# Kernel tuning notes

Hardware: AMD Instinct MI355X
Metric: run time of the kernel (lower is better)

## Reference

```python
import jax, jax.numpy as jnp
import numpy as np

C = 256      # channels
G = 8        # groups
K = 9        # 3x3 sampling points (DCNv4 default kernel_size=3)
DWK = 3      # dw_kernel_size (wrapper passes kernel_size=3)
OFFSET_SCALE = 1.0
N, H, W = 8, 64, 64


def setup_inputs() -> dict:
    key = jax.random.key(0)
    ks = jax.random.split(key, 6)
    def init(k, shape, fan):
        return jax.random.normal(k, shape, jnp.float32) * (fan ** -0.5)
    return {
        "x": jax.random.normal(ks[0], (N, C, H, W), jnp.float32),
        "dw_w": init(ks[1], (C, 1, DWK, DWK), DWK * DWK),   # depthwise conv (OIHW, groups=C)
        "dw_b": jnp.zeros((C,), jnp.float32),
        "om_w": init(ks[2], (G * K * 3, C), C) * 0.01,       # offset/mask linear (small offsets)
        "om_b": jnp.zeros((G * K * 3,), jnp.float32),
        "vp_w": init(ks[3], (C, C), C),                      # value_proj
        "vp_b": jnp.zeros((C,), jnp.float32),
        "op_w": init(ks[4], (C, C), C),                      # output_proj (output_bias=False)
    }


def reference(x, dw_w, dw_b, om_w, om_b, vp_w, vp_b, op_w):
    n, c, h, w = x.shape
    cg = c // G
    L = h * w
    # b c h w -> b (h w) c
    xf = x.transpose(0, 2, 3, 1).reshape(n, L, c)
    value = (xf @ vp_w.T + vp_b).reshape(n, L, G, cg)
    # offset/mask branch: depthwise conv on raw input, then linear
    om_in = jax.lax.conv_general_dilated(
        x, dw_w, (1, 1), "SAME", feature_group_count=c,
        dimension_numbers=("NCHW", "OIHW", "NCHW")) + dw_b[None, :, None, None]
    om = om_in.transpose(0, 2, 3, 1).reshape(n, L, c) @ om_w.T + om_b  # (n, L, G*K*3)
    om = om.reshape(n, h, w, G, K * 3)
    off = om[..., : 2 * K].reshape(n, h, w, G, K, 2) * OFFSET_SCALE     # (dy, dx) per point
    mask = om[..., 2 * K:]                                              # (n,h,w,G,K) raw (DCNv4: no softmax)
    # base 3x3 dilation-1 grid centered at each pixel
    d = jnp.arange(-1, 2, dtype=jnp.float32)
    dy, dx = jnp.meshgrid(d, d, indexing="ij")
    base = jnp.stack([dy.ravel(), dx.ravel()], -1)  # (K, 2)
    py = (jnp.arange(h, dtype=jnp.float32).reshape(1, h, 1, 1, 1)
          + base[:, 0].reshape(1, 1, 1, 1, K) + off[..., 0])  # (n,h,w,G,K)
    px = (jnp.arange(w, dtype=jnp.float32).reshape(1, 1, w, 1, 1)
          + base[:, 1].reshape(1, 1, 1, 1, K) + off[..., 1])
    y0 = jnp.floor(py); x0 = jnp.floor(px)
    ty = py - y0; tx = px - x0
    y0i = y0.astype(jnp.int32); x0i = x0.astype(jnp.int32)

    def gather(yi, xi, wgt):
        valid = (yi >= 0) & (yi < h) & (xi >= 0) & (xi < w)
        idx = jnp.clip(yi, 0, h - 1) * w + jnp.clip(xi, 0, w - 1)       # (n,h,w,G,K)
        idx = idx.transpose(0, 1, 2, 4, 3).reshape(n, L * K, G)[..., None]
        g = jnp.take_along_axis(value, idx, axis=1)                     # (n, L*K, G, cg)
        g = g.reshape(n, h, w, K, G, cg).transpose(0, 1, 2, 4, 3, 5)    # (n,h,w,G,K,cg)
        return g * (wgt * valid)[..., None]

    sampled = (gather(y0i,     x0i,     (1 - ty) * (1 - tx))
             + gather(y0i,     x0i + 1, (1 - ty) * tx)
             + gather(y0i + 1, x0i,     ty * (1 - tx))
             + gather(y0i + 1, x0i + 1, ty * tx))
    out = jnp.einsum("nhwgk,nhwgkc->nhwgc", mask, sampled)  # mask-weighted aggregation
    out = out.reshape(n, L, c) @ op_w.T                      # output_proj (no bias)
    # b (h w) c -> b c h w
    return out.reshape(n, h, w, c).transpose(0, 3, 1, 2)
```

## Files before the change

kernel.cpp:

```cpp
#include <hip/hip_runtime.h>
#include <math.h>

#define N_  8
#define C_  256
#define G_  8
#define CG_ 32
#define K_  9
#define H_  64
#define W_  64
#define L_  (H_*W_)
#define OM_ 216
#define OMP_ 256

using frag_ab = __attribute__((ext_vector_type(8))) short;
using frag_cd = __attribute__((ext_vector_type(4))) float;

__device__ __forceinline__ unsigned short f2bf(float f) {
    unsigned int u = __float_as_uint(f);
    u += 0x7FFFu + ((u >> 16) & 1u);
    return (unsigned short)(u >> 16);
}
__device__ __forceinline__ float bflo(unsigned int u) { return __uint_as_float(u << 16); }
__device__ __forceinline__ float bfhi(unsigned int u) { return __uint_as_float(u & 0xFFFF0000u); }

__device__ __forceinline__ void gld16(const void* g, void* l) {
    __builtin_amdgcn_global_load_lds((const __attribute__((address_space(1))) void*)g,
                                     (__attribute__((address_space(3))) void*)l, 16, 0, 0);
}

__global__ __launch_bounds__(256) void cvt_weights(const float* __restrict__ vp_w,
                                                   const float* __restrict__ om_w,
                                                   const float* __restrict__ om_b,
                                                   const float* __restrict__ op_w,
                                                   unsigned short* __restrict__ vp_wb,
                                                   unsigned short* __restrict__ om_wb,
                                                   float* __restrict__ om_bp,
                                                   unsigned short* __restrict__ op_wb) {
    int idx = blockIdx.x * 256 + threadIdx.x;
    if (idx < C_ * C_) {
        vp_wb[idx] = f2bf(vp_w[idx]);
        op_wb[idx] = f2bf(op_w[idx]);
        om_wb[idx] = (idx < OM_ * C_) ? f2bf(om_w[idx]) : (unsigned short)0;
    }
    if (idx < OMP_) om_bp[idx] = (idx < OM_) ? om_b[idx] : 0.f;
}

__global__ __launch_bounds__(256) void dwt_kernel(const float* __restrict__ x,
                                                  const float* __restrict__ w,
                                                  const float* __restrict__ b,
                                                  unsigned short* __restrict__ omb) {
    const int n = blockIdx.z, y = blockIdx.y, c0 = blockIdx.x * 32;
    const int tid = threadIdx.x;
    __shared__ float xs[3][32][66];
    if (tid < 192) {
        int r = tid / 64, c = (tid / 2) % 32, e = tid & 1;
        xs[r][c][e * 65] = 0.f;
    }
    const float* xb = x + ((size_t)n * C_ + c0) * L_;
    for (int i = tid; i < 3 * 32 * 16; i += 256) {
        int r = i >> 9;
        int rem = i & 511;
        int c = rem >> 4;
        int x4 = (rem & 15) * 4;
        int yy = y + r - 1;
        float4 v = make_float4(0.f, 0.f, 0.f, 0.f);
        if ((unsigned)yy < (unsigned)H_) v = *(const float4*)(xb + (size_t)c * L_ + yy * W_ + x4);
        xs[r][c][1 + x4] = v.x; xs[r][c][2 + x4] = v.y;
        xs[r][c][3 + x4] = v.z; xs[r][c][4 + x4] = v.w;
    }
    __syncthreads();

    const int c = tid & 31, x0 = (tid >> 5) * 8;
    float wv[9];
#pragma unroll
    for (int i = 0; i < 9; i++) wv[i] = w[(c0 + c) * 9 + i];
    const float bias = b[c0 + c];
    float o[8];
#pragma unroll
    for (int j = 0; j < 8; j++) o[j] = bias;
#pragma unroll
    for (int r = 0; r < 3; r++) {
        float v[10];
#pragma unroll
        for (int d = 0; d < 10; d++) v[d] = xs[r][c][x0 + d];
#pragma unroll
        for (int j = 0; j < 8; j++)
            o[j] += wv[r * 3] * v[j] + wv[r * 3 + 1] * v[j + 1] + wv[r * 3 + 2] * v[j + 2];
    }
#pragma unroll
    for (int j = 0; j < 8; j++)
        omb[((size_t)n * L_ + y * W_ + x0 + j) * C_ + c0 + c] = f2bf(o[j]);
}

__global__ __launch_bounds__(256) void xcvt_kernel(const float* __restrict__ x,
                                                   unsigned short* __restrict__ xb) {
    const int n = blockIdx.z, c0 = blockIdx.y * 32, l0 = blockIdx.x * 64;
    const int tid = threadIdx.x;
    __shared__ float t[32][65];
    {
        int c = tid >> 3, l8 = (tid & 7) * 8;
        const float* src = x + ((size_t)n * C_ + c0 + c) * L_ + l0 + l8;
        float4 a = *(const float4*)src;
        float4 d = *(const float4*)(src + 4);
        t[c][l8 + 0] = a.x; t[c][l8 + 1] = a.y; t[c][l8 + 2] = a.z; t[c][l8 + 3] = a.w;
        t[c][l8 + 4] = d.x; t[c][l8 + 5] = d.y; t[c][l8 + 6] = d.z; t[c][l8 + 7] = d.w;
    }
    __syncthreads();
    {
        int l = tid >> 2, cq = (tid & 3) * 8;
        uint4 pk;
        unsigned short* pp = (unsigned short*)&pk;
#pragma unroll
        for (int i = 0; i < 8; i++) pp[i] = f2bf(t[cq + i][l]);
        *(uint4*)(xb + ((size_t)n * L_ + l0 + l) * C_ + c0 + cq) = pk;
    }
}

template <bool BF16_OUT, bool BIAS>
__global__ __launch_bounds__(256) void gemm_bf16(const unsigned short* __restrict__ A,
                                                 const unsigned short* __restrict__ B,
                                                 const float* __restrict__ bias,
                                                 void* __restrict__ Dv,
                                                 int drow, long bbatch, long dbatch) {
    __shared__ unsigned short As[128 * 32];
    __shared__ unsigned short Bs[128 * 32];
    const int tid = threadIdx.x;
    const long i0 = (long)blockIdx.x * 128;
    const long j0 = (long)blockIdx.y * 128;
    const unsigned short* Ab = A + i0 * C_;
    const unsigned short* Bb = B + bbatch * blockIdx.z + j0 * C_;
    const int wave = tid >> 6, lane = tid & 63;
    const int iw = (wave & 1) * 64, jw = (wave >> 1) * 64;
    const int lm = lane & 15, kq = lane >> 4;
    const int srow = tid >> 2, scol = (tid & 3) * 8;

    frag_cd acc[4][4];
#pragma unroll
    for (int a = 0; a < 4; a++)
#pragma unroll
        for (int c = 0; c < 4; c++) acc[a][c] = (frag_cd){0.f, 0.f, 0.f, 0.f};

    for (int k0 = 0; k0 < C_; k0 += 32) {
        const unsigned short* ga0 = Ab + (long)srow * C_ + k0 + scol;
        const unsigned short* gb0 = Bb + (long)srow * C_ + k0 + scol;
        gld16(ga0,            As + tid * 8);
        gld16(ga0 + 64 * C_,  As + 2048 + tid * 8);
        gld16(gb0,            Bs + tid * 8);
        gld16(gb0 + 64 * C_,  Bs + 2048 + tid * 8);
        __syncthreads();
        frag_ab af[4], bfr[4];
#pragma unroll
        for (int mi = 0; mi < 4; mi++)
            af[mi] = *(const frag_ab*)&As[(iw + mi * 16 + lm) * 32 + kq * 8];
#pragma unroll
        for (int ni = 0; ni < 4; ni++)
            bfr[ni] = *(const frag_ab*)&Bs[(jw + ni * 16 + lm) * 32 + kq * 8];
#pragma unroll
        for (int mi = 0; mi < 4; mi++)
#pragma unroll
            for (int ni = 0; ni < 4; ni++)
                acc[mi][ni] = __builtin_amdgcn_mfma_f32_16x16x32_bf16(af[mi], bfr[ni], acc[mi][ni], 0, 0, 0);
        __syncthreads();
    }

    float bv[4];
#pragma unroll
    for (int ni = 0; ni < 4; ni++)
        bv[ni] = BIAS ? bias[(int)(j0 + jw + ni * 16 + lm)] : 0.f;

    const long ibase = i0 + iw + kq * 4;
    const long jbase = j0 + jw + lm;
    const long dz = dbatch * blockIdx.z;
#pragma unroll
    for (int mi = 0; mi < 4; mi++) {
#pragma unroll
        for (int ni = 0; ni < 4; ni++) {
            long j = jbase + ni * 16;
#pragma unroll
            for (int r = 0; r < 4; r++) {
                long i = ibase + mi * 16 + r;
                float v = acc[mi][ni][r] + bv[ni];
                if (BF16_OUT)
                    ((unsigned short*)Dv)[dz + i * drow + j] = f2bf(v);
                else
                    ((float*)Dv)[dz + i * drow + j] = v;
            }
        }
    }
}

__global__ __launch_bounds__(256) void sample_kernel(const unsigned short* __restrict__ value,
                                                     const float* __restrict__ om,
                                                     unsigned short* __restrict__ interm) {
    const int n = blockIdx.y;
    const int l0 = blockIdx.x * 8;
    const int tid = threadIdx.x;
    const int p = tid >> 5;
    const int l = l0 + p;
    const int y = l >> 6, xp = l & 63;
    const int g = (tid >> 2) & 7;
    const int c8 = (tid & 3) * 8;

    __shared__ float sOm[8 * OM_];
    const float* omsrc = om + ((size_t)n * L_ + l0) * OMP_;
    for (int i = tid; i < 8 * OM_; i += 256) {
        int pp = i / OM_;
        int j = i - pp * OM_;
        sOm[i] = omsrc[pp * OMP_ + j];
    }
    __syncthreads();

    const unsigned short* vb = value + (size_t)n * L_ * C_ + g * CG_ + c8;
    const float* so = &sOm[p * OM_ + g * 27];
    float acc[8] = {0.f, 0.f, 0.f, 0.f, 0.f, 0.f, 0.f, 0.f};
#pragma unroll
    for (int k = 0; k < K_; k++) {
        float offy = so[2 * k], offx = so[2 * k + 1], mk = so[18 + k];
        float py = (float)(y + k / 3 - 1) + offy;
        float px = (float)(xp + k % 3 - 1) + offx;
        float fy = floorf(py), fx = floorf(px);
        float ty = py - fy, tx = px - fx;
        int y0 = (int)fy, x0 = (int)fx;
        int y1 = y0 + 1, x1 = x0 + 1;
        float vy0 = ((unsigned)y0 < (unsigned)H_) ? 1.f : 0.f;
        float vy1 = ((unsigned)y1 < (unsigned)H_) ? 1.f : 0.f;
        float vx0 = ((unsigned)x0 < (unsigned)W_) ? 1.f : 0.f;
        float vx1 = ((unsigned)x1 < (unsigned)W_) ? 1.f : 0.f;
        int cy0 = min(max(y0, 0), H_ - 1), cy1 = min(max(y1, 0), H_ - 1);
        int cx0 = min(max(x0, 0), W_ - 1), cx1 = min(max(x1, 0), W_ - 1);
        float w00 = mk * (1.f - ty) * (1.f - tx) * vy0 * vx0;
        float w01 = mk * (1.f - ty) * tx * vy0 * vx1;
        float w10 = mk * ty * (1.f - tx) * vy1 * vx0;
        float w11 = mk * ty * tx * vy1 * vx1;
        const uint4 v00 = *(const uint4*)(vb + (size_t)(cy0 * W_ + cx0) * C_);
        const uint4 v01 = *(const uint4*)(vb + (size_t)(cy0 * W_ + cx1) * C_);
        const uint4 v10 = *(const uint4*)(vb + (size_t)(cy1 * W_ + cx0) * C_);
        const uint4 v11 = *(const uint4*)(vb + (size_t)(cy1 * W_ + cx1) * C_);
#define ACC8(V, WW) { \
        acc[0] += WW * bflo(V.x); acc[1] += WW * bfhi(V.x); \
        acc[2] += WW * bflo(V.y); acc[3] += WW * bfhi(V.y); \
        acc[4] += WW * bflo(V.z); acc[5] += WW * bfhi(V.z); \
        acc[6] += WW * bflo(V.w); acc[7] += WW * bfhi(V.w); }
        ACC8(v00, w00) ACC8(v01, w01) ACC8(v10, w10) ACC8(v11, w11)
#undef ACC8
    }
    uint4 pk;
    unsigned short* pp2 = (unsigned short*)&pk;
#pragma unroll
    for (int i = 0; i < 8; i++) pp2[i] = f2bf(acc[i]);
    *(uint4*)(interm + ((size_t)n * L_ + l) * C_ + g * CG_ + c8) = pk;
}

extern "C" void kernel_launch(void* const* d_in, const int* in_sizes, int n_in,
                              void* d_out, int out_size, void* d_ws, size_t ws_size,
                              hipStream_t stream) {
    const float* x    = (const float*)d_in[0];
    const float* dw_w = (const float*)d_in[1];
    const float* dw_b = (const float*)d_in[2];
    const float* om_w = (const float*)d_in[3];
    const float* om_b = (const float*)d_in[4];
    const float* vp_w = (const float*)d_in[5];
    const float* vp_b = (const float*)d_in[6];
    const float* op_w = (const float*)d_in[7];
    float* out = (float*)d_out;

    char* ws = (char*)d_ws;
    unsigned short* xb      = (unsigned short*)(ws);
    unsigned short* omb     = (unsigned short*)(ws + 16777216);
    unsigned short* valueb  = (unsigned short*)(ws + 33554432);
    float*          omf     = (float*)(ws + 50331648);
    unsigned short* vp_wb   = (unsigned short*)(ws + 83886080);
    unsigned short* om_wb   = (unsigned short*)(ws + 84017152);
    unsigned short* op_wb   = (unsigned short*)(ws + 84148224);
    float*          om_bp   = (float*)(ws + 84279296);
    unsigned short* intermb = xb;

    cvt_weights<<<dim3(256), 256, 0, stream>>>(vp_w, om_w, om_b, op_w,
                                               vp_wb, om_wb, om_bp, op_wb);
    dwt_kernel<<<dim3(C_ / 32, H_, N_), 256, 0, stream>>>(x, dw_w, dw_b, omb);
    xcvt_kernel<<<dim3(L_ / 64, C_ / 32, N_), 256, 0, stream>>>(x, xb);
    gemm_bf16<true, true><<<dim3(256, 2, 1), 256, 0, stream>>>(
        xb, vp_wb, vp_b, valueb, C_, 0, 0);
    gemm_bf16<false, true><<<dim3(256, 2, 1), 256, 0, stream>>>(
        omb, om_wb, om_bp, omf, OMP_, 0, 0);
    sample_kernel<<<dim3(L_ / 8, N_), 256, 0, stream>>>(valueb, omf, intermb);
    gemm_bf16<false, false><<<dim3(2, 32, N_), 256, 0, stream>>>(
        op_wb, intermb, nullptr, out, L_, (long)L_ * C_, (long)C_ * L_);
}
```

Before: 185.1 us.

## Fuse x bf16 transpose into depthwise conv kernel and precompute sampling weights

Merges the x-to-bf16 NHWC conversion into the depthwise conv kernel, reusing the center row already staged in shared memory, and stages both outputs through LDS so they can be written as 16-byte stores. This removes one kernel launch and a second full read of x. The sampling kernel now computes bilinear weights and byte offsets once per (pixel, group, point) into shared memory instead of redundantly in each of the 4 channel lanes, then gathers using those precomputed offsets. The cost is extra shared memory and an additional barrier in both kernels.

```diff
diff --git a/kernel.cpp b/kernel.cpp
--- a/kernel.cpp
+++ b/kernel.cpp
@@ -45,26 +45,25 @@
     if (idx < OMP_) om_bp[idx] = (idx < OM_) ? om_b[idx] : 0.f;
 }
 
-__global__ __launch_bounds__(256) void dwt_kernel(const float* __restrict__ x,
-                                                  const float* __restrict__ w,
-                                                  const float* __restrict__ b,
-                                                  unsigned short* __restrict__ omb) {
+__global__ __launch_bounds__(256) void prep_kernel(const float* __restrict__ x,
+                                                   const float* __restrict__ w,
+                                                   const float* __restrict__ b,
+                                                   unsigned short* __restrict__ xb,
+                                                   unsigned short* __restrict__ omb) {
     const int n = blockIdx.z, y = blockIdx.y, c0 = blockIdx.x * 32;
     const int tid = threadIdx.x;
     __shared__ float xs[3][32][66];
+    __shared__ __align__(16) unsigned short os[2][64][40];
     if (tid < 192) {
         int r = tid / 64, c = (tid / 2) % 32, e = tid & 1;
         xs[r][c][e * 65] = 0.f;
     }
-    const float* xb = x + ((size_t)n * C_ + c0) * L_;
+    const float* xbase = x + ((size_t)n * C_ + c0) * L_;
     for (int i = tid; i < 3 * 32 * 16; i += 256) {
-        int r = i >> 9;
-        int rem = i & 511;
-        int c = rem >> 4;
-        int x4 = (rem & 15) * 4;
+        int r = i >> 9, rem = i & 511, c = rem >> 4, x4 = (rem & 15) * 4;
         int yy = y + r - 1;
         float4 v = make_float4(0.f, 0.f, 0.f, 0.f);
-        if ((unsigned)yy < (unsigned)H_) v = *(const float4*)(xb + (size_t)c * L_ + yy * W_ + x4);
+        if ((unsigned)yy < (unsigned)H_) v = *(const float4*)(xbase + (size_t)c * L_ + yy * W_ + x4);
         xs[r][c][1 + x4] = v.x; xs[r][c][2 + x4] = v.y;
         xs[r][c][3 + x4] = v.z; xs[r][c][4 + x4] = v.w;
     }
@@ -88,32 +87,18 @@
             o[j] += wv[r * 3] * v[j] + wv[r * 3 + 1] * v[j + 1] + wv[r * 3 + 2] * v[j + 2];
     }
 #pragma unroll
-    for (int j = 0; j < 8; j++)
-        omb[((size_t)n * L_ + y * W_ + x0 + j) * C_ + c0 + c] = f2bf(o[j]);
-}
-
-__global__ __launch_bounds__(256) void xcvt_kernel(const float* __restrict__ x,
-                                                   unsigned short* __restrict__ xb) {
-    const int n = blockIdx.z, c0 = blockIdx.y * 32, l0 = blockIdx.x * 64;
-    const int tid = threadIdx.x;
-    __shared__ float t[32][65];
-    {
-        int c = tid >> 3, l8 = (tid & 7) * 8;
-        const float* src = x + ((size_t)n * C_ + c0 + c) * L_ + l0 + l8;
-        float4 a = *(const float4*)src;
-        float4 d = *(const float4*)(src + 4);
-        t[c][l8 + 0] = a.x; t[c][l8 + 1] = a.y; t[c][l8 + 2] = a.z; t[c][l8 + 3] = a.w;
-        t[c][l8 + 4] = d.x; t[c][l8 + 5] = d.y; t[c][l8 + 6] = d.z; t[c][l8 + 7] = d.w;
-    }
-    __syncthreads();
-    {
-        int l = tid >> 2, cq = (tid & 3) * 8;
-        uint4 pk;
-        unsigned short* pp = (unsigned short*)&pk;
-#pragma unroll
-        for (int i = 0; i < 8; i++) pp[i] = f2bf(t[cq + i][l]);
-        *(uint4*)(xb + ((size_t)n * L_ + l0 + l) * C_ + c0 + cq) = pk;
-    }
+    for (int j = 0; j < 8; j++) {
+        os[0][x0 + j][c] = f2bf(xs[1][c][1 + x0 + j]);
+        os[1][x0 + j][c] = f2bf(o[j]);
+    }
+    __syncthreads();
+
+    const int l = tid >> 2, c8 = (tid & 3) * 8;
+    uint4 va = *(const uint4*)&os[0][l][c8];
+    uint4 vc = *(const uint4*)&os[1][l][c8];
+    size_t dst = ((size_t)n * L_ + y * W_ + l) * C_ + c0 + c8;
+    *(uint4*)(xb + dst) = va;
+    *(uint4*)(omb + dst) = vc;
 }
 
 template <bool BF16_OUT, bool BIAS>
@@ -195,60 +180,71 @@
     const int n = blockIdx.y;
     const int l0 = blockIdx.x * 8;
     const int tid = threadIdx.x;
-    const int p = tid >> 5;
-    const int l = l0 + p;
-    const int y = l >> 6, xp = l & 63;
-    const int g = (tid >> 2) & 7;
-    const int c8 = (tid & 3) * 8;
 
     __shared__ float sOm[8 * OM_];
+    __shared__ float4 wgt[64][9];
+    __shared__ uint4  soff[64][9];
+
     const float* omsrc = om + ((size_t)n * L_ + l0) * OMP_;
     for (int i = tid; i < 8 * OM_; i += 256) {
         int pp = i / OM_;
-        int j = i - pp * OM_;
-        sOm[i] = omsrc[pp * OMP_ + j];
-    }
-    __syncthreads();
-
-    const unsigned short* vb = value + (size_t)n * L_ * C_ + g * CG_ + c8;
-    const float* so = &sOm[p * OM_ + g * 27];
-    float acc[8] = {0.f, 0.f, 0.f, 0.f, 0.f, 0.f, 0.f, 0.f};
-#pragma unroll
-    for (int k = 0; k < K_; k++) {
+        sOm[i] = omsrc[pp * OMP_ + (i - pp * OM_)];
+    }
+    __syncthreads();
+
+    for (int it = tid; it < 576; it += 256) {
+        int pair = it / 9, k = it - pair * 9;
+        int p = pair >> 3, g = pair & 7;
+        int l = l0 + p, y = l >> 6, xp2 = l & 63;
+        const float* so = &sOm[p * OM_ + g * 27];
         float offy = so[2 * k], offx = so[2 * k + 1], mk = so[18 + k];
         float py = (float)(y + k / 3 - 1) + offy;
-        float px = (float)(xp + k % 3 - 1) + offx;
+        float px = (float)(xp2 + k % 3 - 1) + offx;
         float fy = floorf(py), fx = floorf(px);
         float ty = py - fy, tx = px - fx;
-        int y0 = (int)fy, x0 = (int)fx;
-        int y1 = y0 + 1, x1 = x0 + 1;
+        int y0 = (int)fy, x0i = (int)fx;
+        int y1 = y0 + 1, x1 = x0i + 1;
         float vy0 = ((unsigned)y0 < (unsigned)H_) ? 1.f : 0.f;
         float vy1 = ((unsigned)y1 < (unsigned)H_) ? 1.f : 0.f;
-        float vx0 = ((unsigned)x0 < (unsigned)W_) ? 1.f : 0.f;
+        float vx0 = ((unsigned)x0i < (unsigned)W_) ? 1.f : 0.f;
         float vx1 = ((unsigned)x1 < (unsigned)W_) ? 1.f : 0.f;
         int cy0 = min(max(y0, 0), H_ - 1), cy1 = min(max(y1, 0), H_ - 1);
-        int cx0 = min(max(x0, 0), W_ - 1), cx1 = min(max(x1, 0), W_ - 1);
-        float w00 = mk * (1.f - ty) * (1.f - tx) * vy0 * vx0;
-        float w01 = mk * (1.f - ty) * tx * vy0 * vx1;
-        float w10 = mk * ty * (1.f - tx) * vy1 * vx0;
-        float w11 = mk * ty * tx * vy1 * vx1;
-        const uint4 v00 = *(const uint4*)(vb + (size_t)(cy0 * W_ + cx0) * C_);
-        const uint4 v01 = *(const uint4*)(vb + (size_t)(cy0 * W_ + cx1) * C_);
-        const uint4 v10 = *(const uint4*)(vb + (size_t)(cy1 * W_ + cx0) * C_);
-        const uint4 v11 = *(const uint4*)(vb + (size_t)(cy1 * W_ + cx1) * C_);
+        int cx0 = min(max(x0i, 0), W_ - 1), cx1 = min(max(x1, 0), W_ - 1);
+        wgt[pair][k] = make_float4(mk * (1.f - ty) * (1.f - tx) * vy0 * vx0,
+                                   mk * (1.f - ty) * tx         * vy0 * vx1,
+                                   mk * ty         * (1.f - tx) * vy1 * vx0,
+                                   mk * ty         * tx         * vy1 * vx1);
+        soff[pair][k] = make_uint4((unsigned)((cy0 * W_ + cx0) << 9),
+                                   (unsigned)((cy0 * W_ + cx1) << 9),
+                                   (unsigned)((cy1 * W_ + cx0) << 9),
+                                   (unsigned)((cy1 * W_ + cx1) << 9));
+    }
+    __syncthreads();
+
+    const int pair = tid >> 2, p = pair >> 3, g = pair & 7, c8 = (tid & 3) * 8;
+    const char* vb = (const char*)(value + (size_t)n * L_ * C_ + g * CG_ + c8);
+    float acc[8] = {0.f, 0.f, 0.f, 0.f, 0.f, 0.f, 0.f, 0.f};
+#pragma unroll
+    for (int k = 0; k < K_; k++) {
+        float4 wk = wgt[pair][k];
+        uint4  ok = soff[pair][k];
+        const uint4 v00 = *(const uint4*)(vb + ok.x);
+        const uint4 v01 = *(const uint4*)(vb + ok.y);
+        const uint4 v10 = *(const uint4*)(vb + ok.z);
+        const uint4 v11 = *(const uint4*)(vb + ok.w);
 #define ACC8(V, WW) { \
         acc[0] += WW * bflo(V.x); acc[1] += WW * bfhi(V.x); \
         acc[2] += WW * bflo(V.y); acc[3] += WW * bfhi(V.y); \
         acc[4] += WW * bflo(V.z); acc[5] += WW * bfhi(V.z); \
         acc[6] += WW * bflo(V.w); acc[7] += WW * bfhi(V.w); }
-        ACC8(v00, w00) ACC8(v01, w01) ACC8(v10, w10) ACC8(v11, w11)
+        ACC8(v00, wk.x) ACC8(v01, wk.y) ACC8(v10, wk.z) ACC8(v11, wk.w)
 #undef ACC8
     }
     uint4 pk;
     unsigned short* pp2 = (unsigned short*)&pk;
 #pragma unroll
     for (int i = 0; i < 8; i++) pp2[i] = f2bf(acc[i]);
-    *(uint4*)(interm + ((size_t)n * L_ + l) * C_ + g * CG_ + c8) = pk;
+    *(uint4*)(interm + ((size_t)n * L_ + l0 + p) * C_ + g * CG_ + c8) = pk;
 }
 
 extern "C" void kernel_launch(void* const* d_in, const int* in_sizes, int n_in,
@@ -277,8 +273,7 @@
 
     cvt_weights<<<dim3(256), 256, 0, stream>>>(vp_w, om_w, om_b, op_w,
                                                vp_wb, om_wb, om_bp, op_wb);
-    dwt_kernel<<<dim3(C_ / 32, H_, N_), 256, 0, stream>>>(x, dw_w, dw_b, omb);
-    xcvt_kernel<<<dim3(L_ / 64, C_ / 32, N_), 256, 0, stream>>>(x, xb);
+    prep_kernel<<<dim3(C_ / 32, H_, N_), 256, 0, stream>>>(x, dw_w, dw_b, xb, omb);
     gemm_bf16<true, true><<<dim3(256, 2, 1), 256, 0, stream>>>(
         xb, vp_wb, vp_b, valueb, C_, 0, 0);
     gemm_bf16<false, true><<<dim3(256, 2, 1), 256, 0, stream>>>(
```

After: 176.4 us. 1.05x faster.
